# Kernel optimization log

Measured on AMD Instinct MI355X. Metric: run time of the kernel, lower is better.

The kernel has to match this reference:

```python
import jax, jax.numpy as jnp
import numpy as np

LOG2PI = 1.8378770664093453  # log(2*pi)


def _pixel_positions(d, h, w):
    # centered coordinates, stacked as (x, y, z) per the torch module
    z = jnp.arange(d, dtype=jnp.float32) - (d - 1) / 2.0
    y = jnp.arange(h, dtype=jnp.float32) - (h - 1) / 2.0
    x = jnp.arange(w, dtype=jnp.float32) - (w - 1) / 2.0
    zz = jnp.broadcast_to(z[:, None, None], (d, h, w))
    yy = jnp.broadcast_to(y[None, :, None], (d, h, w))
    xx = jnp.broadcast_to(x[None, None, :], (d, h, w))
    return jnp.stack([xx, yy, zz], axis=-1).reshape(-1, 3)  # (N, 3)


def setup_inputs() -> dict:
    key = jax.random.key(0)
    k0, k1, k2, k3, k4 = jax.random.split(key, 5)
    B, D = 512, 256
    d, h, w = 16, 64, 64
    scale = 1.0 / np.sqrt(D)
    return {
        "representation": jax.random.normal(k0, (B, D), dtype=jnp.float32),
        "mean_w": jax.random.normal(k1, (3, D), dtype=jnp.float32) * scale,
        "mean_b": jax.random.normal(k2, (3,), dtype=jnp.float32) * 0.1,
        "scale_w": jax.random.normal(k3, (6, D), dtype=jnp.float32) * scale,
        "scale_b": jax.random.normal(k4, (6,), dtype=jnp.float32) * 0.1,
        "pixel_positions": _pixel_positions(d, h, w),
    }


def reference(representation, mean_w, mean_b, scale_w, scale_b, pixel_positions):
    # linear heads
    means = representation @ mean_w.T + mean_b            # (B, 3)
    s_raw = representation @ scale_w.T + scale_b          # (B, 6)
    s = jax.nn.elu(s_raw) + 1.0                           # (B, 6)

    # FillScaleTriL with SoftplusTransform on the diagonal.
    # tril_indices(3,3) row-major order: (0,0),(1,0),(1,1),(2,0),(2,1),(2,2)
    l00 = jax.nn.softplus(s[:, 0])
    l10 = s[:, 1]
    l11 = jax.nn.softplus(s[:, 2])
    l20 = s[:, 3]
    l21 = s[:, 4]
    l22 = jax.nn.softplus(s[:, 5])

    # Mahalanobis term via analytic forward-substitution of L z = (x - mu)
    diff = pixel_positions[None, :, :] - means[:, None, :]  # (B, N, 3)
    z0 = diff[..., 0] / l00[:, None]
    z1 = (diff[..., 1] - l10[:, None] * z0) / l11[:, None]
    z2 = (diff[..., 2] - l20[:, None] * z0 - l21[:, None] * z1) / l22[:, None]
    maha = z0 * z0 + z1 * z1 + z2 * z2                     # (B, N)

    log_det = jnp.log(l00) + jnp.log(l11) + jnp.log(l22)   # (B,)
    log_probs = -0.5 * maha - 1.5 * LOG2PI - log_det[:, None]  # (B, N)

    # stable normalize over the pixel grid (matches torch code incl. eps)
    lp = log_probs - jnp.max(log_probs, axis=1, keepdims=True)
    p = jnp.exp(lp)
    return p / (jnp.sum(p, axis=1, keepdims=True) + 1e-10)
```

## Files before the change

### kernel.cpp

```cpp
#include <hip/hip_runtime.h>
#include <math.h>


#define LOG2PI_F 1.8378770664093453f

__device__ __forceinline__ float waveMax(float v) {
#pragma unroll
    for (int off = 32; off; off >>= 1) v = fmaxf(v, __shfl_xor(v, off, 64));
    return v;
}
__device__ __forceinline__ float waveSum(float v) {
#pragma unroll
    for (int off = 32; off; off >>= 1) v += __shfl_xor(v, off, 64);
    return v;
}

__global__ __launch_bounds__(1024, 4)
void mvn_profile_kernel(const float* __restrict__ rep,
                        const float* __restrict__ mean_w,
                        const float* __restrict__ mean_b,
                        const float* __restrict__ scale_w,
                        const float* __restrict__ scale_b,
                        float* __restrict__ out)
{
    const int b    = blockIdx.x;
    const int tid  = threadIdx.x;
    const int lane = tid & 63;
    const int wave = tid >> 6;

    __shared__ float s_dots[9];
    __shared__ float s_params[10];
    __shared__ float s_red[16];
    __shared__ float s_bcast;

    if (wave < 9) {
        const float4* r4 = (const float4*)(rep + (size_t)b * 256);
        const float*  wrow = (wave < 3) ? (mean_w + wave * 256)
                                        : (scale_w + (wave - 3) * 256);
        const float4* w4 = (const float4*)wrow;
        float4 a = r4[lane];
        float4 w = w4[lane];
        float d = a.x * w.x + a.y * w.y + a.z * w.z + a.w * w.w;
        d = waveSum(d);
        if (lane == 0) s_dots[wave] = d;
    }
    __syncthreads();

    if (tid == 0) {
        float mx = s_dots[0] + mean_b[0];
        float my = s_dots[1] + mean_b[1];
        float mz = s_dots[2] + mean_b[2];
        float s[6];
#pragma unroll
        for (int j = 0; j < 6; j++) {
            float x = s_dots[3 + j] + scale_b[j];
            s[j] = (x > 0.0f) ? (x + 1.0f) : (expm1f(x) + 1.0f);
        }
        float l00 = fmaxf(s[0], 0.0f) + log1pf(expf(-fabsf(s[0])));
        float l10 = s[1];
        float l11 = fmaxf(s[2], 0.0f) + log1pf(expf(-fabsf(s[2])));
        float l20 = s[3];
        float l21 = s[4];
        float l22 = fmaxf(s[5], 0.0f) + log1pf(expf(-fabsf(s[5])));
        s_params[0] = mx;
        s_params[1] = my;
        s_params[2] = mz;
        s_params[3] = 1.0f / l00;
        s_params[4] = l10;
        s_params[5] = 1.0f / l11;
        s_params[6] = l20;
        s_params[7] = l21;
        s_params[8] = 1.0f / l22;
        s_params[9] = -1.5f * LOG2PI_F - (logf(l00) + logf(l11) + logf(l22));
    }
    __syncthreads();

    const float mx  = s_params[0], my  = s_params[1], mz  = s_params[2];
    const float i00 = s_params[3], l10 = s_params[4], i11 = s_params[5];
    const float l20 = s_params[6], l21 = s_params[7], i22 = s_params[8];
    const float cb  = s_params[9];

    const float py = (float)(tid >> 4) - 31.5f;
    const float dy = py - my;

    float cc[4];
    float e2[4];
#pragma unroll
    for (int j = 0; j < 4; j++) {
        float px = (float)(((tid * 4) & 63) + j) - 31.5f;
        float dx = px - mx;
        float z0 = dx * i00;
        float z1 = (dy - l10 * z0) * i11;
        float c2 = mz + l20 * z0 + l21 * z1;
        e2[j] = c2 * i22;
        cc[j] = cb - 0.5f * (z0 * z0 + z1 * z1);
    }

    float lpv[64];
    float tmax = -INFINITY;
#pragma unroll
    for (int k = 0; k < 16; k++) {
        float t = ((float)k - 7.5f) * i22;
#pragma unroll
        for (int j = 0; j < 4; j++) {
            float z2 = t - e2[j];
            float lp = cc[j] - 0.5f * z2 * z2;
            lpv[k * 4 + j] = lp;
            tmax = fmaxf(tmax, lp);
        }
    }

    tmax = waveMax(tmax);
    if (lane == 0) s_red[wave] = tmax;
    __syncthreads();
    if (wave == 0) {
        float v = (lane < 16) ? s_red[lane] : -INFINITY;
        v = waveMax(v);
        if (lane == 0) s_bcast = v;
    }
    __syncthreads();
    const float m = s_bcast;

    float tsum = 0.0f;
#pragma unroll
    for (int i = 0; i < 64; i++) {
        float p = __expf(lpv[i] - m);
        lpv[i] = p;
        tsum += p;
    }
    tsum = waveSum(tsum);
    __syncthreads();
    if (lane == 0) s_red[wave] = tsum;
    __syncthreads();
    if (wave == 0) {
        float v = (lane < 16) ? s_red[lane] : 0.0f;
        v = waveSum(v);
        if (lane == 0) s_bcast = 1.0f / (v + 1e-10f);
    }
    __syncthreads();
    const float r = s_bcast;

    float* orow = out + (size_t)b * 65536 + (size_t)tid * 4;
#pragma unroll
    for (int k = 0; k < 16; k++) {
        float4 o;
        o.x = lpv[k * 4 + 0] * r;
        o.y = lpv[k * 4 + 1] * r;
        o.z = lpv[k * 4 + 2] * r;
        o.w = lpv[k * 4 + 3] * r;
        *(float4*)(orow + (size_t)k * 4096) = o;
    }
}

extern "C" void kernel_launch(void* const* d_in, const int* in_sizes, int n_in,
                              void* d_out, int out_size, void* d_ws, size_t ws_size,
                              hipStream_t stream) {
    const float* rep     = (const float*)d_in[0];
    const float* mean_w  = (const float*)d_in[1];
    const float* mean_b  = (const float*)d_in[2];
    const float* scale_w = (const float*)d_in[3];
    const float* scale_b = (const float*)d_in[4];
    float* out = (float*)d_out;

    const int B = in_sizes[0] / 256;
    hipLaunchKernelGGL(mvn_profile_kernel, dim3(B), dim3(1024), 0, stream,
                       rep, mean_w, mean_b, scale_w, scale_b, out);
}
```

Baseline: 155.6 us.

## Replace max reduction with analytic grid-point shift and recompute exps

Drops the block-wide max reduction and instead finds analytically the grid voxel nearest the mode by rounding during forward substitution. Its Mahalanobis value serves as the stabilising shift, and the constant log-det term cancels in the normalisation. The exp values are no longer held in a 64-register array; they are recomputed in the store loop, which frees registers for higher occupancy (launch bounds raised to 8). The cost is twice the exp2 work, plus a possible loss of precision if the rounded voxel is not the true maximum.

```diff
diff --git a/kernel.cpp b/kernel.cpp
--- a/kernel.cpp
+++ b/kernel.cpp
@@ -2,20 +2,16 @@
 #include <math.h>
 
 
-#define LOG2PI_F 1.8378770664093453f
+#define HL2E 0.7213475204444817f
+#define L2E  1.4426950408889634f
 
-__device__ __forceinline__ float waveMax(float v) {
-#pragma unroll
-    for (int off = 32; off; off >>= 1) v = fmaxf(v, __shfl_xor(v, off, 64));
-    return v;
-}
 __device__ __forceinline__ float waveSum(float v) {
 #pragma unroll
     for (int off = 32; off; off >>= 1) v += __shfl_xor(v, off, 64);
     return v;
 }
 
-__global__ __launch_bounds__(1024, 4)
+__global__ __launch_bounds__(1024, 8)
 void mvn_profile_kernel(const float* __restrict__ rep,
                         const float* __restrict__ mean_w,
                         const float* __restrict__ mean_b,
@@ -62,28 +58,34 @@
         float l20 = s[3];
         float l21 = s[4];
         float l22 = fmaxf(s[5], 0.0f) + log1pf(expf(-fabsf(s[5])));
-        s_params[0] = mx;
-        s_params[1] = my;
-        s_params[2] = mz;
-        s_params[3] = 1.0f / l00;
-        s_params[4] = l10;
-        s_params[5] = 1.0f / l11;
-        s_params[6] = l20;
-        s_params[7] = l21;
-        s_params[8] = 1.0f / l22;
-        s_params[9] = -1.5f * LOG2PI_F - (logf(l00) + logf(l11) + logf(l22));
+        float i00 = 1.0f / l00, i11 = 1.0f / l11, i22 = 1.0f / l22;
+
+        float gx = fminf(fmaxf(roundf(mx + 31.5f), 0.0f), 63.0f) - 31.5f;
+        float z0 = (gx - mx) * i00;
+        float ty = my + l10 * z0;
+        float gy = fminf(fmaxf(roundf(ty + 31.5f), 0.0f), 63.0f) - 31.5f;
+        float z1 = ((gy - my) - l10 * z0) * i11;
+        float tz = mz + l20 * z0 + l21 * z1;
+        float gz = fminf(fmaxf(roundf(tz + 7.5f), 0.0f), 15.0f) - 7.5f;
+        float z2 = ((gz - mz) - l20 * z0 - l21 * z1) * i22;
+        float mahag = z0 * z0 + z1 * z1 + z2 * z2;
+
+        s_params[0] = mx;  s_params[1] = my;  s_params[2] = mz;
+        s_params[3] = i00; s_params[4] = l10; s_params[5] = i11;
+        s_params[6] = l20; s_params[7] = l21; s_params[8] = i22;
+        s_params[9] = HL2E * mahag;
     }
     __syncthreads();
 
     const float mx  = s_params[0], my  = s_params[1], mz  = s_params[2];
     const float i00 = s_params[3], l10 = s_params[4], i11 = s_params[5];
     const float l20 = s_params[6], l21 = s_params[7], i22 = s_params[8];
-    const float cb  = s_params[9];
+    const float sc2 = s_params[9];
 
     const float py = (float)(tid >> 4) - 31.5f;
     const float dy = py - my;
 
-    float cc[4];
+    float cc2[4];
     float e2[4];
 #pragma unroll
     for (int j = 0; j < 4; j++) {
@@ -91,45 +93,22 @@
         float dx = px - mx;
         float z0 = dx * i00;
         float z1 = (dy - l10 * z0) * i11;
-        float c2 = mz + l20 * z0 + l21 * z1;
-        e2[j] = c2 * i22;
-        cc[j] = cb - 0.5f * (z0 * z0 + z1 * z1);
+        e2[j]  = (mz + l20 * z0 + l21 * z1) * i22;
+        cc2[j] = sc2 - HL2E * (z0 * z0 + z1 * z1);
     }
 
-    float lpv[64];
-    float tmax = -INFINITY;
+    float tsum = 0.0f;
 #pragma unroll
     for (int k = 0; k < 16; k++) {
         float t = ((float)k - 7.5f) * i22;
 #pragma unroll
         for (int j = 0; j < 4; j++) {
             float z2 = t - e2[j];
-            float lp = cc[j] - 0.5f * z2 * z2;
-            lpv[k * 4 + j] = lp;
-            tmax = fmaxf(tmax, lp);
+            float q  = fmaf(z2 * z2, -HL2E, cc2[j]);
+            tsum += exp2f(q);
         }
     }
-
-    tmax = waveMax(tmax);
-    if (lane == 0) s_red[wave] = tmax;
-    __syncthreads();
-    if (wave == 0) {
-        float v = (lane < 16) ? s_red[lane] : -INFINITY;
-        v = waveMax(v);
-        if (lane == 0) s_bcast = v;
-    }
-    __syncthreads();
-    const float m = s_bcast;
-
-    float tsum = 0.0f;
-#pragma unroll
-    for (int i = 0; i < 64; i++) {
-        float p = __expf(lpv[i] - m);
-        lpv[i] = p;
-        tsum += p;
-    }
     tsum = waveSum(tsum);
-    __syncthreads();
     if (lane == 0) s_red[wave] = tsum;
     __syncthreads();
     if (wave == 0) {
@@ -143,11 +122,24 @@
     float* orow = out + (size_t)b * 65536 + (size_t)tid * 4;
 #pragma unroll
     for (int k = 0; k < 16; k++) {
+        float t = ((float)k - 7.5f) * i22;
         float4 o;
-        o.x = lpv[k * 4 + 0] * r;
-        o.y = lpv[k * 4 + 1] * r;
-        o.z = lpv[k * 4 + 2] * r;
-        o.w = lpv[k * 4 + 3] * r;
+        {
+            float z2 = t - e2[0];
+            o.x = exp2f(fmaf(z2 * z2, -HL2E, cc2[0])) * r;
+        }
+        {
+            float z2 = t - e2[1];
+            o.y = exp2f(fmaf(z2 * z2, -HL2E, cc2[1])) * r;
+        }
+        {
+            float z2 = t - e2[2];
+            o.z = exp2f(fmaf(z2 * z2, -HL2E, cc2[2])) * r;
+        }
+        {
+            float z2 = t - e2[3];
+            o.w = exp2f(fmaf(z2 * z2, -HL2E, cc2[3])) * r;
+        }
         *(float4*)(orow + (size_t)k * 4096) = o;
     }
 }
```

Result: slower. 167.7 us (+7.8%).
